# Performance work log

Hardware: AMD Instinct MI355X
Metric: run time of the kernel (lower is better)

The kernel has to match this reference:

```python
import jax, jax.numpy as jnp
import numpy as np
import math

B, N, M, C, H = 4, 2048, 2048, 512, 4
D_V = C // H          # 128, used for scale and value head dim
D_QK = 2 * C // H     # 256, q/k head dim due to seq-axis split of the 2*dim qkv output
SCALE = D_V ** -0.5
EPS = 1e-12           # F.normalize eps


def _l2norm(t):
    n = jnp.linalg.norm(t, axis=-1, keepdims=True)
    return t / jnp.maximum(n, EPS)


def setup_inputs() -> dict:
    key = jax.random.key(0)
    k1, k2, k3, k4 = jax.random.split(key, 4)
    x = jax.random.normal(k1, (B, N, C), dtype=jnp.float32)
    context = jax.random.normal(k2, (B, M, C), dtype=jnp.float32)
    W_qkv = jax.random.normal(k3, (2 * C, C), dtype=jnp.float32) * 0.02  # torch Linear weight [out,in]
    W_proj = jax.random.normal(k4, (C, C), dtype=jnp.float32) * 0.02
    radius = jnp.ones((H,), dtype=jnp.float32) * math.sqrt(D_V)
    return {"x": x, "context": context, "W_qkv": W_qkv, "W_proj": W_proj, "radius": radius}


def reference(x, context, W_qkv, W_proj, radius):
    # qkv(cat([x, context], dim=1)) then split along sequence: q from x rows, k from context rows
    q = jnp.einsum('bnc,oc->bno', x, W_qkv)        # [B,N,2C]
    k = jnp.einsum('bmc,oc->bmo', context, W_qkv)  # [B,M,2C]
    q = q.reshape(B, N, H, D_QK).transpose(0, 2, 1, 3)       # [B,H,N,256]
    k = k.reshape(B, M, H, D_QK).transpose(0, 2, 1, 3)       # [B,H,M,256]
    v = context.reshape(B, M, H, D_V).transpose(0, 2, 1, 3)  # [B,H,M,128]
    r = radius[None, :, None, None]
    q = _l2norm(q) * r
    k = _l2norm(k) * r
    attn = jnp.einsum('bhnd,bhmd->bhnm', q, k) * SCALE
    attn = jax.nn.softmax(attn, axis=-1)
    out = jnp.einsum('bhnm,bhmd->bhnd', attn, v)
    out = out.transpose(0, 2, 1, 3).reshape(B, N, C)
    return jnp.einsum('bnc,oc->bno', out, W_proj)
```

## Files before the change

### kernel.cpp

```cpp
#include <hip/hip_runtime.h>
#include <hip/hip_bf16.h>
#include <stdint.h>

#define SCALE_F 0.08838834764831845f

typedef __attribute__((ext_vector_type(8))) short short8;
typedef __attribute__((ext_vector_type(4))) float f32x4;
typedef __attribute__((ext_vector_type(16))) float f32x16;
typedef __attribute__((ext_vector_type(2))) unsigned int uint2v;

__device__ __forceinline__ void g2l16(const void* g, void* l) {
  __builtin_amdgcn_global_load_lds(
      (const __attribute__((address_space(1))) void*)g,
      (__attribute__((address_space(3))) void*)l, 16, 0, 0);
}

__device__ __forceinline__ unsigned pkbf(float a, float b) {
  union { __hip_bfloat16 h[2]; unsigned u; } o;
  o.h[0] = __float2bfloat16(a); o.h[1] = __float2bfloat16(b);
  return o.u;
}

__global__ __launch_bounds__(256) void convert_all(
    const float* __restrict__ x, const float* __restrict__ ctx,
    const float* __restrict__ wqkv, const float* __restrict__ wproj,
    __hip_bfloat16* __restrict__ ab, __hip_bfloat16* __restrict__ wb,
    __hip_bfloat16* __restrict__ wpb)
{
  size_t qi = (size_t)blockIdx.x * 256 + threadIdx.x;
  const float* src; __hip_bfloat16* dst; size_t off;
  if (qi < 1048576)      { src = x;     dst = ab;           off = qi; }
  else if (qi < 2097152) { src = ctx;   dst = ab + 4194304; off = qi - 1048576; }
  else if (qi < 2228224) { src = wqkv;  dst = wb;           off = qi - 2097152; }
  else                   { src = wproj; dst = wpb;          off = qi - 2228224; }
  float4 v = ((const float4*)src)[off];
  union { __hip_bfloat16 h4[4]; uint2 u; } o;
  o.h4[0] = __float2bfloat16(v.x); o.h4[1] = __float2bfloat16(v.y);
  o.h4[2] = __float2bfloat16(v.z); o.h4[3] = __float2bfloat16(v.w);
  ((uint2*)dst)[off] = o.u;
}

__global__ __launch_bounds__(256) void transpose_v(
    const float* __restrict__ ctx, __hip_bfloat16* __restrict__ vt)
{
  __shared__ float tile[128][33];
  const int bid = blockIdx.x;
  const int mt = bid & 63;
  const int bh = bid >> 6;
  const int h = bh & 3, b = bh >> 2;
  const int tid = threadIdx.x;
  for (int i = 0; i < 16; ++i) {
    int idx = i * 256 + tid;
    int mm = idx >> 7, d = idx & 127;
    tile[d][mm] = ctx[((size_t)b * 2048 + mt * 32 + mm) * 512 + h * 128 + d];
  }
  __syncthreads();
  for (int i = 0; i < 16; ++i) {
    int idx = i * 256 + tid;
    int d = idx >> 5, mm = idx & 31;
    vt[((size_t)bh * 128 + d) * 2048 + mt * 32 + mm] = __float2bfloat16(tile[d][mm]);
  }
}

__global__ __launch_bounds__(256) void gemm_qkv(
    const __hip_bfloat16* __restrict__ A,
    const __hip_bfloat16* __restrict__ Bw,
    const float* __restrict__ radius,
    __hip_bfloat16* __restrict__ qn, __hip_bfloat16* __restrict__ kn)
{
  __shared__ __hip_bfloat16 sAB[384 * 32];
  __hip_bfloat16* sA = sAB;
  __hip_bfloat16* sB = sAB + 128 * 32;
  const int tid = threadIdx.x;
  const int wave = tid >> 6, lane = tid & 63;
  const int ln = lane & 15, q4 = lane >> 4;
  const int ro = blockIdx.x >> 2;
  const int co = blockIdx.x & 3;
  const __hip_bfloat16* Ab = A + (size_t)ro * 128 * 512;
  const __hip_bfloat16* Bb = Bw + (size_t)co * 256 * 512;
  const int row0 = tid >> 2, p0 = tid & 3;
  f32x4 acc[2][16] = {};
  for (int k0 = 0; k0 < 512; k0 += 32) {
    for (int i = 0; i < 2; ++i)
      g2l16(Ab + (size_t)(i * 64 + row0) * 512 + k0 + p0 * 8,
            (char*)sA + (i * 256 + tid) * 16);
    for (int i = 0; i < 4; ++i)
      g2l16(Bb + (size_t)(i * 64 + row0) * 512 + k0 + p0 * 8,
            (char*)sB + (i * 256 + tid) * 16);
    __syncthreads();
    short8 af0 = *(const short8*)(sA + (wave * 32 + ln) * 32 + q4 * 8);
    short8 af1 = *(const short8*)(sA + (wave * 32 + 16 + ln) * 32 + q4 * 8);
#pragma unroll
    for (int ni = 0; ni < 16; ++ni) {
      short8 bf = *(const short8*)(sB + (ni * 16 + ln) * 32 + q4 * 8);
      acc[0][ni] = __builtin_amdgcn_mfma_f32_16x16x32_bf16(af0, bf, acc[0][ni], 0, 0, 0);
      acc[1][ni] = __builtin_amdgcn_mfma_f32_16x16x32_bf16(af1, bf, acc[1][ni], 0, 0, 0);
    }
    __syncthreads();
  }
  float scl[2][4];
  const float rad = radius[co];
  const int grow0 = ro * 128;
  const bool isq = grow0 < 8192;
  const int rl = isq ? grow0 : grow0 - 8192;
  const float qfac = isq ? rad * rad * SCALE_F : 1.0f;
#pragma unroll
  for (int mi = 0; mi < 2; ++mi)
#pragma unroll
    for (int r = 0; r < 4; ++r) {
      float ss = 0.f;
#pragma unroll
      for (int ni = 0; ni < 16; ++ni) { float v = acc[mi][ni][r]; ss += v * v; }
      ss += __shfl_xor(ss, 1); ss += __shfl_xor(ss, 2);
      ss += __shfl_xor(ss, 4); ss += __shfl_xor(ss, 8);
      scl[mi][r] = qfac / fmaxf(sqrtf(ss), 1e-12f);
    }
  __hip_bfloat16* dstT = (isq ? qn : kn) +
      ((size_t)((rl >> 11) * 4 + co) * 2048 + (rl & 2047)) * 256;
  __hip_bfloat16* sEw = sAB + wave * 3072;
#pragma unroll
  for (int c = 0; c < 4; ++c) {
    int mi = c >> 1, hh = c & 1;
    if ((q4 >> 1) == hh) {
      int lr = (q4 & 1) * 4;
#pragma unroll
      for (int r = 0; r < 4; ++r)
#pragma unroll
        for (int ni = 0; ni < 16; ++ni)
          sEw[(lr + r) * 264 + ni * 16 + ln] =
              __float2bfloat16(acc[mi][ni][r] * scl[mi][r]);
    }
    asm volatile("s_waitcnt lgkmcnt(0)" ::: "memory");
#pragma unroll
    for (int p = 0; p < 4; ++p) {
      int idx = p * 64 + lane;
      int rr = idx >> 5, c8 = idx & 31;
      short8 v = *(const short8*)(sEw + rr * 264 + c8 * 8);
      *(short8*)(dstT + (size_t)(wave * 32 + c * 8 + rr) * 256 + c8 * 8) = v;
    }
    asm volatile("s_waitcnt lgkmcnt(0)" ::: "memory");
  }
}

__global__ __launch_bounds__(256) void gemm_nt(
    const __hip_bfloat16* __restrict__ A, const __hip_bfloat16* __restrict__ B,
    float* __restrict__ C, int O, int K, int tiles_o)
{
  __shared__ __hip_bfloat16 sA[128 * 32];
  __shared__ __hip_bfloat16 sB[128 * 32];
  const int tid = threadIdx.x;
  const int wave = tid >> 6, lane = tid & 63;
  const int ln = lane & 15, q = lane >> 4;
  const int br = (blockIdx.x / tiles_o) * 128;
  const int bo = (blockIdx.x % tiles_o) * 128;
  const int wr = (wave >> 1) * 64, wc = (wave & 1) * 64;
  const __hip_bfloat16* Ab = A + (size_t)br * K;
  const __hip_bfloat16* Bb = B + (size_t)bo * K;
  const int row0 = tid >> 2, p0 = tid & 3;
  f32x4 acc[4][4] = {};
  for (int k0 = 0; k0 < K; k0 += 32) {
    for (int i = 0; i < 2; ++i) {
      int row = i * 64 + row0;
      g2l16(Ab + (size_t)row * K + k0 + p0 * 8, (char*)sA + (i * 256 + tid) * 16);
      g2l16(Bb + (size_t)row * K + k0 + p0 * 8, (char*)sB + (i * 256 + tid) * 16);
    }
    __syncthreads();
    short8 af[4], bfr[4];
    for (int mi = 0; mi < 4; ++mi)
      af[mi] = *(const short8*)(sA + (wr + mi * 16 + ln) * 32 + q * 8);
    for (int ni = 0; ni < 4; ++ni)
      bfr[ni] = *(const short8*)(sB + (wc + ni * 16 + ln) * 32 + q * 8);
    for (int mi = 0; mi < 4; ++mi)
      for (int ni = 0; ni < 4; ++ni)
        acc[mi][ni] = __builtin_amdgcn_mfma_f32_16x16x32_bf16(af[mi], bfr[ni], acc[mi][ni], 0, 0, 0);
    __syncthreads();
  }
  for (int mi = 0; mi < 4; ++mi)
    for (int ni = 0; ni < 4; ++ni) {
      int rg = br + wr + mi * 16 + q * 4;
      int cg = bo + wc + ni * 16 + ln;
      for (int r = 0; r < 4; ++r)
        C[(size_t)(rg + r) * O + cg] = acc[mi][ni][r];
    }
}

__global__ __launch_bounds__(256, 2) void attn(
    const __hip_bfloat16* __restrict__ qn,
    const __hip_bfloat16* __restrict__ kn,
    const __hip_bfloat16* __restrict__ vt,
    float* __restrict__ Op,
    float* __restrict__ den)
{
  __shared__ __hip_bfloat16 sK[2][32 * 256];
  __shared__ __hip_bfloat16 sV[2][128 * 32];
  const int tid = threadIdx.x, wave = tid >> 6, lane = tid & 63;
  const int m32 = lane & 31, hi = lane >> 5;
  const int i = blockIdx.x;
  const int bh = (i & 7) + 8 * ((i >> 3) & 1);
  const int half = (i >> 4) & 1;
  const int nt = i >> 5;
  const int mbase = half * 1024;
  const __hip_bfloat16* Q = qn + ((size_t)bh * 2048 + nt * 128 + wave * 32) * 256;
  const __hip_bfloat16* Kp = kn + (size_t)bh * 2048 * 256;
  const __hip_bfloat16* Vp = vt + (size_t)bh * 128 * 2048;

  short8 qf[16];
  for (int kk = 0; kk < 16; ++kk)
    qf[kk] = *(const short8*)(Q + m32 * 256 + kk * 16 + hi * 8);

  f32x16 oacc[4];
  for (int v = 0; v < 4; ++v)
    for (int j = 0; j < 16; ++j) oacc[v][j] = 0.f;
  float denom = 0.f;

  for (int t = 0; t < 4; ++t) {
    int D = t * 256 + tid, row = D >> 5, cc = D & 31;
    g2l16(Kp + (size_t)(mbase + row) * 256 + ((cc ^ (row & 7)) << 3),
          (char*)sK[0] + D * 16);
  }
  for (int t = 0; t < 2; ++t) {
    int D = t * 256 + tid, rd = D >> 2, cc = D & 3;
    g2l16(Vp + (size_t)rd * 2048 + mbase + ((cc ^ ((rd >> 1) & 3)) << 3),
          (char*)sV[0] + D * 16);
  }
  __syncthreads();

  for (int it = 0; it < 32; ++it) {
    const int cur = it & 1, nxt = cur ^ 1;
    if (it + 1 < 32) {
      const int m1 = mbase + (it + 1) * 32;
      for (int t = 0; t < 4; ++t) {
        int D = t * 256 + tid, row = D >> 5, cc = D & 31;
        g2l16(Kp + (size_t)(m1 + row) * 256 + ((cc ^ (row & 7)) << 3),
              (char*)sK[nxt] + D * 16);
      }
      for (int t = 0; t < 2; ++t) {
        int D = t * 256 + tid, rd = D >> 2, cc = D & 3;
        g2l16(Vp + (size_t)rd * 2048 + m1 + ((cc ^ ((rd >> 1) & 3)) << 3),
              (char*)sV[nxt] + D * 16);
      }
    }
    const __hip_bfloat16* sKc = sK[cur];
    f32x16 sa, sb;
    for (int j = 0; j < 16; ++j) { sa[j] = 0.f; sb[j] = 0.f; }
#pragma unroll
    for (int kk = 0; kk < 8; ++kk) {
      int ca = kk * 2 + hi, cb = (kk + 8) * 2 + hi;
      short8 kfa = *(const short8*)(sKc + m32 * 256 + ((ca ^ (m32 & 7)) << 3));
      short8 kfb = *(const short8*)(sKc + m32 * 256 + ((cb ^ (m32 & 7)) << 3));
      sa = __builtin_amdgcn_mfma_f32_32x32x16_bf16(kfa, qf[kk], sa, 0, 0, 0);
      sb = __builtin_amdgcn_mfma_f32_32x32x16_bf16(kfb, qf[kk + 8], sb, 0, 0, 0);
    }
    union { unsigned u[4]; short8 s; } ua, ub;
    {
      float e0, e1, e2, e3;
      unsigned u0, u1, u2, u3;
      e0 = __expf(sa[0] + sb[0]); e1 = __expf(sa[1] + sb[1]);
      e2 = __expf(sa[2] + sb[2]); e3 = __expf(sa[3] + sb[3]);
      denom += (e0 + e1) + (e2 + e3);
      u0 = pkbf(e0, e1); u1 = pkbf(e2, e3);
      e0 = __expf(sa[4] + sb[4]); e1 = __expf(sa[5] + sb[5]);
      e2 = __expf(sa[6] + sb[6]); e3 = __expf(sa[7] + sb[7]);
      denom += (e0 + e1) + (e2 + e3);
      u2 = pkbf(e0, e1); u3 = pkbf(e2, e3);
      uint2v s0 = __builtin_amdgcn_permlane32_swap(u0, u2, false, false);
      uint2v s1 = __builtin_amdgcn_permlane32_swap(u1, u3, false, false);
      ua.u[0] = s0.x; ua.u[1] = s1.x; ua.u[2] = s0.y; ua.u[3] = s1.y;
      e0 = __expf(sa[8] + sb[8]);   e1 = __expf(sa[9] + sb[9]);
      e2 = __expf(sa[10] + sb[10]); e3 = __expf(sa[11] + sb[11]);
      denom += (e0 + e1) + (e2 + e3);
      u0 = pkbf(e0, e1); u1 = pkbf(e2, e3);
      e0 = __expf(sa[12] + sb[12]); e1 = __expf(sa[13] + sb[13]);
      e2 = __expf(sa[14] + sb[14]); e3 = __expf(sa[15] + sb[15]);
      denom += (e0 + e1) + (e2 + e3);
      u2 = pkbf(e0, e1); u3 = pkbf(e2, e3);
      uint2v s2 = __builtin_amdgcn_permlane32_swap(u0, u2, false, false);
      uint2v s3 = __builtin_amdgcn_permlane32_swap(u1, u3, false, false);
      ub.u[0] = s2.x; ub.u[1] = s3.x; ub.u[2] = s2.y; ub.u[3] = s3.y;
    }
    const __hip_bfloat16* sVc = sV[cur];
#pragma unroll
    for (int kc = 0; kc < 2; ++kc) {
      short8 pf = kc ? ub.s : ua.s;
#pragma unroll
      for (int vi = 0; vi < 4; ++vi) {
        int rd = vi * 32 + m32;
        int c = kc * 2 + hi;
        short8 vf = *(const short8*)(sVc + rd * 32 + ((c ^ ((rd >> 1) & 3)) << 3));
        oacc[vi] = __builtin_amdgcn_mfma_f32_32x32x16_bf16(vf, pf, oacc[vi], 0, 0, 0);
      }
    }
    __syncthreads();
  }

  float dfull = denom + __shfl_xor(denom, 32);
  float* Opb = Op + (size_t)(half * 16 + bh) * 2048 * 128;
  float* denb = den + (size_t)(half * 16 + bh) * 2048;
  const int rbase = nt * 128 + wave * 32;
  if (hi == 0) denb[rbase + m32] = dfull;
  float* sc_ = (float*)(&sK[0][0]) + wave * 1056;
#pragma unroll
  for (int vi = 0; vi < 4; ++vi) {
#pragma unroll
    for (int reg = 0; reg < 16; ++reg) {
      int dL = (reg & 3) + 8 * (reg >> 2) + 4 * hi;
      sc_[m32 * 33 + dL] = oacc[vi][reg];
    }
    asm volatile("s_waitcnt lgkmcnt(0)" ::: "memory");
#pragma unroll
    for (int qq = 0; qq < 16; ++qq) {
      int qr = qq * 2 + hi;
      Opb[(size_t)(rbase + qr) * 128 + vi * 32 + m32] = sc_[qr * 33 + m32];
    }
    asm volatile("s_waitcnt lgkmcnt(0)" ::: "memory");
  }
}

__global__ __launch_bounds__(256) void combine(
    const float* __restrict__ Op, const float* __restrict__ den,
    __hip_bfloat16* __restrict__ ob)
{
  int qi = blockIdx.x * 256 + threadIdx.x;
  int r = qi >> 5;
  int dq = qi & 31;
  int bh = r >> 11, n = r & 2047, b = bh >> 2, h = bh & 3;
  float4 o0 = ((const float4*)Op)[qi];
  float4 o1 = ((const float4*)(Op + 4194304))[qi];
  float inv = 1.0f / (den[r] + den[32768 + r]);
  union { __hip_bfloat16 h4[4]; uint2 u; } o;
  o.h4[0] = __float2bfloat16((o0.x + o1.x) * inv);
  o.h4[1] = __float2bfloat16((o0.y + o1.y) * inv);
  o.h4[2] = __float2bfloat16((o0.z + o1.z) * inv);
  o.h4[3] = __float2bfloat16((o0.w + o1.w) * inv);
  *(uint2*)&ob[((size_t)b * 2048 + n) * 512 + h * 128 + dq * 4] = o.u;
}

extern "C" void kernel_launch(void* const* d_in, const int* in_sizes, int n_in,
                              void* d_out, int out_size, void* d_ws, size_t ws_size,
                              hipStream_t stream) {
  const float* x      = (const float*)d_in[0];
  const float* ctx    = (const float*)d_in[1];
  const float* wqkv   = (const float*)d_in[2];
  const float* wproj  = (const float*)d_in[3];
  const float* radius = (const float*)d_in[4];
  char* ws = (char*)d_ws;
  __hip_bfloat16* ab  = (__hip_bfloat16*)(ws);
  __hip_bfloat16* wb  = (__hip_bfloat16*)(ws + 16777216);
  __hip_bfloat16* wpb = (__hip_bfloat16*)(ws + 17825792);
  float*          Op  = (float*)(ws + 18350080);
  float*          den = (float*)(ws + 18350080 + 33554432);
  __hip_bfloat16* qn  = (__hip_bfloat16*)(ws + 85458944);
  __hip_bfloat16* kn  = (__hip_bfloat16*)(ws + 102236160);
  __hip_bfloat16* vt  = (__hip_bfloat16*)(ws + 119013376);
  __hip_bfloat16* ob  = (__hip_bfloat16*)(ws + 127401984);
  float* out = (float*)d_out;

  convert_all<<<8960, 256, 0, stream>>>(x, ctx, wqkv, wproj, ab, wb, wpb);
  transpose_v<<<1024, 256, 0, stream>>>(ctx, vt);
  gemm_qkv<<<512, 256, 0, stream>>>(ab, wb, radius, qn, kn);
  attn<<<512, 256, 0, stream>>>(qn, kn, vt, Op, den);
  combine<<<4096, 256, 0, stream>>>(Op, den, ob);
  gemm_nt<<<256, 256, 0, stream>>>(ob, wpb, out, 512, 512, 4);
}
```

Before: 227.2 us.

## Fuse context bf16 conversion into V transpose, halve QKV tile, use exp2

```diff
diff --git a/kernel.cpp b/kernel.cpp
--- a/kernel.cpp
+++ b/kernel.cpp
@@ -3,6 +3,7 @@
 #include <stdint.h>
 
 #define SCALE_F 0.08838834764831845f
+#define LOG2E_F 1.4426950408889634f
 
 typedef __attribute__((ext_vector_type(8))) short short8;
 typedef __attribute__((ext_vector_type(4))) float f32x4;
@@ -22,17 +23,16 @@
 }
 
 __global__ __launch_bounds__(256) void convert_all(
-    const float* __restrict__ x, const float* __restrict__ ctx,
-    const float* __restrict__ wqkv, const float* __restrict__ wproj,
+    const float* __restrict__ x, const float* __restrict__ wqkv,
+    const float* __restrict__ wproj,
     __hip_bfloat16* __restrict__ ab, __hip_bfloat16* __restrict__ wb,
     __hip_bfloat16* __restrict__ wpb)
 {
   size_t qi = (size_t)blockIdx.x * 256 + threadIdx.x;
   const float* src; __hip_bfloat16* dst; size_t off;
-  if (qi < 1048576)      { src = x;     dst = ab;           off = qi; }
-  else if (qi < 2097152) { src = ctx;   dst = ab + 4194304; off = qi - 1048576; }
-  else if (qi < 2228224) { src = wqkv;  dst = wb;           off = qi - 2097152; }
-  else                   { src = wproj; dst = wpb;          off = qi - 2228224; }
+  if (qi < 1048576)      { src = x;     dst = ab;  off = qi; }
+  else if (qi < 1179648) { src = wqkv;  dst = wb;  off = qi - 1048576; }
+  else                   { src = wproj; dst = wpb; off = qi - 1179648; }
   float4 v = ((const float4*)src)[off];
   union { __hip_bfloat16 h4[4]; uint2 u; } o;
   o.h4[0] = __float2bfloat16(v.x); o.h4[1] = __float2bfloat16(v.y);
@@ -41,7 +41,8 @@
 }
 
 __global__ __launch_bounds__(256) void transpose_v(
-    const float* __restrict__ ctx, __hip_bfloat16* __restrict__ vt)
+    const float* __restrict__ ctx, __hip_bfloat16* __restrict__ vt,
+    __hip_bfloat16* __restrict__ abctx)
 {
   __shared__ float tile[128][33];
   const int bid = blockIdx.x;
@@ -60,6 +61,12 @@
     int d = idx >> 5, mm = idx & 31;
     vt[((size_t)bh * 128 + d) * 2048 + mt * 32 + mm] = __float2bfloat16(tile[d][mm]);
   }
+  for (int i = 0; i < 16; ++i) {
+    int idx = i * 256 + tid;
+    int mm = idx >> 7, d = idx & 127;
+    abctx[((size_t)b * 2048 + mt * 32 + mm) * 512 + h * 128 + d] =
+        __float2bfloat16(tile[d][mm]);
+  }
 }
 
 __global__ __launch_bounds__(256) void gemm_qkv(
@@ -70,65 +77,59 @@
 {
   __shared__ __hip_bfloat16 sAB[384 * 32];
   __hip_bfloat16* sA = sAB;
-  __hip_bfloat16* sB = sAB + 128 * 32;
+  __hip_bfloat16* sB = sAB + 64 * 32;
   const int tid = threadIdx.x;
   const int wave = tid >> 6, lane = tid & 63;
   const int ln = lane & 15, q4 = lane >> 4;
   const int ro = blockIdx.x >> 2;
   const int co = blockIdx.x & 3;
-  const __hip_bfloat16* Ab = A + (size_t)ro * 128 * 512;
+  const __hip_bfloat16* Ab = A + (size_t)ro * 64 * 512;
   const __hip_bfloat16* Bb = Bw + (size_t)co * 256 * 512;
   const int row0 = tid >> 2, p0 = tid & 3;
-  f32x4 acc[2][16] = {};
+  f32x4 acc[16] = {};
   for (int k0 = 0; k0 < 512; k0 += 32) {
-    for (int i = 0; i < 2; ++i)
-      g2l16(Ab + (size_t)(i * 64 + row0) * 512 + k0 + p0 * 8,
-            (char*)sA + (i * 256 + tid) * 16);
+    g2l16(Ab + (size_t)row0 * 512 + k0 + p0 * 8, (char*)sA + tid * 16);
+#pragma unroll
     for (int i = 0; i < 4; ++i)
       g2l16(Bb + (size_t)(i * 64 + row0) * 512 + k0 + p0 * 8,
             (char*)sB + (i * 256 + tid) * 16);
     __syncthreads();
-    short8 af0 = *(const short8*)(sA + (wave * 32 + ln) * 32 + q4 * 8);
-    short8 af1 = *(const short8*)(sA + (wave * 32 + 16 + ln) * 32 + q4 * 8);
+    short8 af = *(const short8*)(sA + (wave * 16 + ln) * 32 + q4 * 8);
 #pragma unroll
     for (int ni = 0; ni < 16; ++ni) {
       short8 bf = *(const short8*)(sB + (ni * 16 + ln) * 32 + q4 * 8);
-      acc[0][ni] = __builtin_amdgcn_mfma_f32_16x16x32_bf16(af0, bf, acc[0][ni], 0, 0, 0);
-      acc[1][ni] = __builtin_amdgcn_mfma_f32_16x16x32_bf16(af1, bf, acc[1][ni], 0, 0, 0);
-    }
-    __syncthreads();
-  }
-  float scl[2][4];
+      acc[ni] = __builtin_amdgcn_mfma_f32_16x16x32_bf16(af, bf, acc[ni], 0, 0, 0);
+    }
+    __syncthreads();
+  }
   const float rad = radius[co];
-  const int grow0 = ro * 128;
+  const int grow0 = ro * 64;
   const bool isq = grow0 < 8192;
   const int rl = isq ? grow0 : grow0 - 8192;
-  const float qfac = isq ? rad * rad * SCALE_F : 1.0f;
-#pragma unroll
-  for (int mi = 0; mi < 2; ++mi)
-#pragma unroll
-    for (int r = 0; r < 4; ++r) {
-      float ss = 0.f;
-#pragma unroll
-      for (int ni = 0; ni < 16; ++ni) { float v = acc[mi][ni][r]; ss += v * v; }
-      ss += __shfl_xor(ss, 1); ss += __shfl_xor(ss, 2);
-      ss += __shfl_xor(ss, 4); ss += __shfl_xor(ss, 8);
-      scl[mi][r] = qfac / fmaxf(sqrtf(ss), 1e-12f);
-    }
+  const float qfac = isq ? rad * rad * SCALE_F * LOG2E_F : 1.0f;
+  float scl[4];
+#pragma unroll
+  for (int r = 0; r < 4; ++r) {
+    float ss = 0.f;
+#pragma unroll
+    for (int ni = 0; ni < 16; ++ni) { float v = acc[ni][r]; ss += v * v; }
+    ss += __shfl_xor(ss, 1); ss += __shfl_xor(ss, 2);
+    ss += __shfl_xor(ss, 4); ss += __shfl_xor(ss, 8);
+    scl[r] = qfac / fmaxf(sqrtf(ss), 1e-12f);
+  }
   __hip_bfloat16* dstT = (isq ? qn : kn) +
       ((size_t)((rl >> 11) * 4 + co) * 2048 + (rl & 2047)) * 256;
   __hip_bfloat16* sEw = sAB + wave * 3072;
 #pragma unroll
-  for (int c = 0; c < 4; ++c) {
-    int mi = c >> 1, hh = c & 1;
-    if ((q4 >> 1) == hh) {
+  for (int c = 0; c < 2; ++c) {
+    if ((q4 >> 1) == c) {
       int lr = (q4 & 1) * 4;
 #pragma unroll
       for (int r = 0; r < 4; ++r)
 #pragma unroll
         for (int ni = 0; ni < 16; ++ni)
           sEw[(lr + r) * 264 + ni * 16 + ln] =
-              __float2bfloat16(acc[mi][ni][r] * scl[mi][r]);
+              __float2bfloat16(acc[ni][r] * scl[r]);
     }
     asm volatile("s_waitcnt lgkmcnt(0)" ::: "memory");
 #pragma unroll
@@ -136,7 +137,7 @@
       int idx = p * 64 + lane;
       int rr = idx >> 5, c8 = idx & 31;
       short8 v = *(const short8*)(sEw + rr * 264 + c8 * 8);
-      *(short8*)(dstT + (size_t)(wave * 32 + c * 8 + rr) * 256 + c8 * 8) = v;
+      *(short8*)(dstT + (size_t)(wave * 16 + c * 8 + rr) * 256 + c8 * 8) = v;
     }
     asm volatile("s_waitcnt lgkmcnt(0)" ::: "memory");
   }
@@ -255,23 +256,23 @@
     {
       float e0, e1, e2, e3;
       unsigned u0, u1, u2, u3;
-      e0 = __expf(sa[0] + sb[0]); e1 = __expf(sa[1] + sb[1]);
-      e2 = __expf(sa[2] + sb[2]); e3 = __expf(sa[3] + sb[3]);
+      e0 = __builtin_exp2f(sa[0] + sb[0]); e1 = __builtin_exp2f(sa[1] + sb[1]);
+      e2 = __builtin_exp2f(sa[2] + sb[2]); e3 = __builtin_exp2f(sa[3] + sb[3]);
       denom += (e0 + e1) + (e2 + e3);
       u0 = pkbf(e0, e1); u1 = pkbf(e2, e3);
-      e0 = __expf(sa[4] + sb[4]); e1 = __expf(sa[5] + sb[5]);
-      e2 = __expf(sa[6] + sb[6]); e3 = __expf(sa[7] + sb[7]);
+      e0 = __builtin_exp2f(sa[4] + sb[4]); e1 = __builtin_exp2f(sa[5] + sb[5]);
+      e2 = __builtin_exp2f(sa[6] + sb[6]); e3 = __builtin_exp2f(sa[7] + sb[7]);
       denom += (e0 + e1) + (e2 + e3);
       u2 = pkbf(e0, e1); u3 = pkbf(e2, e3);
       uint2v s0 = __builtin_amdgcn_permlane32_swap(u0, u2, false, false);
       uint2v s1 = __builtin_amdgcn_permlane32_swap(u1, u3, false, false);
       ua.u[0] = s0.x; ua.u[1] = s1.x; ua.u[2] = s0.y; ua.u[3] = s1.y;
-      e0 = __expf(sa[8] + sb[8]);   e1 = __expf(sa[9] + sb[9]);
-      e2 = __expf(sa[10] + sb[10]); e3 = __expf(sa[11] + sb[11]);
+      e0 = __builtin_exp2f(sa[8] + sb[8]);   e1 = __builtin_exp2f(sa[9] + sb[9]);
+      e2 = __builtin_exp2f(sa[10] + sb[10]); e3 = __builtin_exp2f(sa[11] + sb[11]);
       denom += (e0 + e1) + (e2 + e3);
       u0 = pkbf(e0, e1); u1 = pkbf(e2, e3);
-      e0 = __expf(sa[12] + sb[12]); e1 = __expf(sa[13] + sb[13]);
-      e2 = __expf(sa[14] + sb[14]); e3 = __expf(sa[15] + sb[15]);
+      e0 = __builtin_exp2f(sa[12] + sb[12]); e1 = __builtin_exp2f(sa[13] + sb[13]);
+      e2 = __builtin_exp2f(sa[14] + sb[14]); e3 = __builtin_exp2f(sa[15] + sb[15]);
       denom += (e0 + e1) + (e2 + e3);
       u2 = pkbf(e0, e1); u3 = pkbf(e2, e3);
       uint2v s2 = __builtin_amdgcn_permlane32_swap(u0, u2, false, false);
@@ -355,9 +356,9 @@
   __hip_bfloat16* ob  = (__hip_bfloat16*)(ws + 127401984);
   float* out = (float*)d_out;
 
-  convert_all<<<8960, 256, 0, stream>>>(x, ctx, wqkv, wproj, ab, wb, wpb);
-  transpose_v<<<1024, 256, 0, stream>>>(ctx, vt);
-  gemm_qkv<<<512, 256, 0, stream>>>(ab, wb, radius, qn, kn);
+  convert_all<<<4864, 256, 0, stream>>>(x, wqkv, wproj, ab, wb, wpb);
+  transpose_v<<<1024, 256, 0, stream>>>(ctx, vt, ab + 4194304);
+  gemm_qkv<<<1024, 256, 0, stream>>>(ab, wb, radius, qn, kn);
   attn<<<512, 256, 0, stream>>>(qn, kn, vt, Op, den);
   combine<<<4096, 256, 0, stream>>>(Op, den, ob);
   gemm_nt<<<256, 256, 0, stream>>>(ob, wpb, out, 512, 512, 4);
```

Result: faster. 218.5 us (-3.8%).
